# Optimization experiments

Hardware: AMD Instinct MI355X
Metric: run time of the kernel (lower is better)

Reference implementation:

```python
import jax, jax.numpy as jnp
import numpy as np

SIGMA = 0.1  # init kwarg sigma
B_CONST = 1.0  # init kwarg b
EPS = 1e-5


def setup_inputs() -> dict:
    key = jax.random.key(0)
    k1, k2 = jax.random.split(key)
    shape = (4, 256, 48, 48)  # N, C, H, W
    return {
        "featureT": jax.random.normal(k1, shape, dtype=jnp.float32),
        "featureI": jax.random.normal(k2, shape, dtype=jnp.float32),
    }


def reference(featureT, featureI):
    # center both features by the target's per-channel mean (over N, H, W)
    meanT = featureT.mean(axis=(0, 2, 3), keepdims=True)
    fI = featureI - meanT
    fT = featureT - meanT
    # l2-normalize channelwise (dim=1)
    fI = fI / jnp.linalg.norm(fI, axis=1, keepdims=True)
    fT = fT / jnp.linalg.norm(fT, axis=1, keepdims=True)
    N, C, H, W = fT.shape
    P = H * W
    # per-sample all-pairs patch cosine similarity: dist[n,p,h,w] = sum_c fT[n,c,p] * fI[n,c,h,w]
    # (equivalent to the per-sample F.conv2d with 1x1 filters from patch_decomposition)
    dist = jnp.einsum('ncp,nchw->nphw', fT.reshape(N, C, P), fI)  # [N, P, H, W]
    raw_dist = (1.0 - dist) / 2.0
    # relative distances along the patch axis (axis=1)
    div = jnp.min(raw_dist, axis=1, keepdims=True)
    relative_dist = raw_dist / (div + EPS)
    # contextual similarity: exp-weighted normalization along axis=1
    Wmat = jnp.exp((B_CONST - relative_dist) / SIGMA)
    CX = Wmat / jnp.sum(Wmat, axis=1, keepdims=True)
    # max over spatial dims (3 then 2), mean over patches
    CX = CX.max(axis=(2, 3))  # [N, P]
    CX = CX.mean(axis=1)      # [N]
    CX_B = -jnp.log(CX)       # [N]
    loss = jnp.mean(CX_B)
    return (loss, CX_B)
```

## Files before the change

### kernel.cpp

```cpp
#include <hip/hip_runtime.h>
#include <hip/hip_fp16.h>

#define NN 4
#define CC 256
#define PP 2304
#define EPSV 1e-5f

typedef __attribute__((ext_vector_type(8))) short bf16x8;
typedef __attribute__((ext_vector_type(4))) float f32x4;

struct alignas(8) h4 { __half2 a, b; };

__device__ inline unsigned fenc(float f) {
  unsigned b = __float_as_uint(f);
  return (b & 0x80000000u) ? ~b : (b | 0x80000000u);
}
__device__ inline float fdec(unsigned e) {
  unsigned b = (e & 0x80000000u) ? (e ^ 0x80000000u) : ~e;
  return __uint_as_float(b);
}

__device__ inline unsigned short f2bf(float x) {
  unsigned u = __float_as_uint(x);
  unsigned r = (u + 0x7FFFu + ((u >> 16) & 1u)) >> 16;
  return (unsigned short)r;
}

__device__ inline void gload_lds16(const unsigned short* g, unsigned short* l) {
  __builtin_amdgcn_global_load_lds(
      (const __attribute__((address_space(1))) void*)g,
      (__attribute__((address_space(3))) void*)l, 16, 0, 0);
}

__global__ __launch_bounds__(256) void k_mean(const float* __restrict__ fT,
                                              float* __restrict__ meanT,
                                              unsigned* __restrict__ divu,
                                              unsigned* __restrict__ M,
                                              float* __restrict__ cxsum) {
  int c = blockIdx.x, t = threadIdx.x;
  float s = 0.f;
  for (int n = 0; n < NN; n++) {
    const float* base = fT + (size_t)n * CC * PP + (size_t)c * PP;
    for (int p = t; p < PP; p += 256) s += base[p];
  }
  for (int o = 32; o > 0; o >>= 1) s += __shfl_down(s, o);
  __shared__ float red[4];
  if ((t & 63) == 0) red[t >> 6] = s;
  __syncthreads();
  if (t == 0) meanT[c] = (red[0] + red[1] + red[2] + red[3]) / (float)(NN * PP);
  if (t < 36) {
    int idx = c * 36 + t;
    divu[idx] = 0xFFFFFFFFu;
    M[idx] = 0u;
  }
  if (blockIdx.x == 0 && t < 4) cxsum[t] = 0.f;
}

__global__ __launch_bounds__(256) void k_norm(const float* __restrict__ fT,
                                              const float* __restrict__ fI,
                                              const float* __restrict__ meanT,
                                              unsigned short* __restrict__ A,
                                              unsigned short* __restrict__ B) {
  int n = blockIdx.y;
  int p0 = blockIdx.x * 16;
  int t = threadIdx.x;
  int tc = t >> 4, tp = t & 15;
  __shared__ float cT[16][257];
  __shared__ float cI[16][257];
  __shared__ float redT[16][17], redI[16][17];
  __shared__ float inv[2][16];
  float aT = 0.f, aI = 0.f;
  int p = p0 + tp;
  for (int c0 = 0; c0 < CC; c0 += 16) {
    int c = c0 + tc;
    float m = meanT[c];
    size_t g = (size_t)n * CC * PP + (size_t)c * PP + p;
    float vT = fT[g] - m;
    float vI = fI[g] - m;
    cT[tp][c] = vT; cI[tp][c] = vI;
    aT += vT * vT; aI += vI * vI;
  }
  redT[tp][tc] = aT; redI[tp][tc] = aI;
  __syncthreads();
  if (t < 16) {
    float sT = 0.f, sI = 0.f;
    for (int k = 0; k < 16; k++) { sT += redT[t][k]; sI += redI[t][k]; }
    inv[0][t] = 1.0f / sqrtf(sT);
    inv[1][t] = 1.0f / sqrtf(sI);
  }
  __syncthreads();
#pragma unroll
  for (int it = 0; it < 2; it++) {
    int task = it * 256 + t;
    int ps = task >> 5;
    int ch = task & 31;
    float iA = inv[0][ps], iB = inv[1][ps];
    unsigned short va[8], vb[8];
#pragma unroll
    for (int e = 0; e < 8; e++) {
      va[e] = f2bf(cT[ps][ch * 8 + e] * iA);
      vb[e] = f2bf(cI[ps][ch * 8 + e] * iB);
    }
    size_t o = ((size_t)(n * PP + p0 + ps)) * CC + ch * 8;
    *(int4*)(A + o) = *(const int4*)va;
    *(int4*)(B + o) = *(const int4*)vb;
  }
}

__global__ __launch_bounds__(256) void k_gemm(const unsigned short* __restrict__ A,
                                              const unsigned short* __restrict__ B,
                                              __half* __restrict__ rawt,
                                              unsigned* __restrict__ divu) {
  int n  = blockIdx.z;
  int i0 = blockIdx.y * 128;
  int j0 = blockIdx.x * 128;
  int t  = threadIdx.x;
  int lane = t & 63;
  int w = t >> 6;
  int wi = w >> 1, wj = w & 1;
  int lr = lane & 15, lq = lane >> 4;

  __shared__ __align__(16) char smem[33792];
  unsigned short* As = (unsigned short*)smem;
  unsigned short* Bs = (unsigned short*)(smem + 16384);
  __half* r16t = (__half*)smem;
  __shared__ unsigned cmin[128];
  if (t < 128) cmin[t] = 0xFFFFFFFFu;

  f32x4 acc[4][4];
#pragma unroll
  for (int a = 0; a < 4; a++)
#pragma unroll
    for (int b = 0; b < 4; b++) acc[a][b] = (f32x4){0.f, 0.f, 0.f, 0.f};

  const size_t baseA = ((size_t)(n * PP + i0)) * CC;
  const size_t baseB = ((size_t)(n * PP + j0)) * CC;
  int lrow8 = lane >> 3;
  int lseg  = (lane & 7) ^ (lrow8 & 7);

  for (int k0 = 0; k0 < CC; k0 += 64) {
    if (k0) __syncthreads();
#pragma unroll
    for (int it = 0; it < 4; it++) {
      int sb = (w * 4 + it) * 64;
      int row = (w * 4 + it) * 8 + lrow8;
      gload_lds16(A + baseA + (size_t)row * CC + k0 + lseg * 8, As + sb * 8);
      gload_lds16(B + baseB + (size_t)row * CC + k0 + lseg * 8, Bs + sb * 8);
    }
    __syncthreads();
#pragma unroll
    for (int ks = 0; ks < 2; ks++) {
      bf16x8 af[4], bf[4];
#pragma unroll
      for (int ti = 0; ti < 4; ti++) {
        int row = wi * 64 + ti * 16 + lr;
        int slot = row * 8 + ((ks * 4 + lq) ^ (lr & 7));
        af[ti] = *(const bf16x8*)&As[slot * 8];
      }
#pragma unroll
      for (int tj = 0; tj < 4; tj++) {
        int row = wj * 64 + tj * 16 + lr;
        int slot = row * 8 + ((ks * 4 + lq) ^ (lr & 7));
        bf[tj] = *(const bf16x8*)&Bs[slot * 8];
      }
#pragma unroll
      for (int ti = 0; ti < 4; ti++)
#pragma unroll
        for (int tj = 0; tj < 4; tj++)
          acc[ti][tj] = __builtin_amdgcn_mfma_f32_16x16x32_bf16(af[ti], bf[tj], acc[ti][tj], 0, 0, 0);
    }
  }

  __syncthreads();
#pragma unroll
  for (int tj = 0; tj < 4; tj++) {
    float mx = -1e30f;
    int cj = wj * 64 + tj * 16 + lr;
#pragma unroll
    for (int ti = 0; ti < 4; ti++) {
      alignas(8) unsigned short pk[4];
#pragma unroll
      for (int r = 0; r < 4; r++) {
        float g = acc[ti][tj][r];
        mx = fmaxf(mx, g);
        pk[r] = __half_as_ushort(__float2half((1.0f - g) * 0.5f));
      }
      int ci = wi * 64 + ti * 16 + lq * 4;
      *(short4*)&r16t[cj * 132 + ci] = *(const short4*)pk;
    }
    atomicMin(&cmin[cj], fenc((1.0f - mx) * 0.5f));
  }
  __syncthreads();
#pragma unroll
  for (int m = 0; m < 8; m++) {
    int chunk = m * 256 + t;
    int row = chunk >> 4, cs = chunk & 15;
    int2 lo = *(const int2*)&r16t[row * 132 + cs * 8];
    int2 hi = *(const int2*)&r16t[row * 132 + cs * 8 + 4];
    int4 v = {lo.x, lo.y, hi.x, hi.y};
    *(int4*)(rawt + ((size_t)(n * PP + j0 + row)) * PP + i0 + cs * 8) = v;
  }
  if (t < 128) atomicMin(&divu[n * PP + j0 + t], cmin[t]);
}

__global__ __launch_bounds__(256) void k_colsum(const __half* __restrict__ rawt,
                                                const unsigned* __restrict__ divu,
                                                float* __restrict__ S) {
  int t = threadIdx.x, lane = t & 63, w = t >> 6;
  int r = blockIdx.x * 4 + w;
  float d = fdec(divu[r]);
  float sc = -10.0f / (d + EPSV);
  const __half* rp = rawt + (size_t)r * PP;
  float s = 0.f;
#pragma unroll
  for (int c = 0; c < 9; c++) {
    h4 hv = *(const h4*)(rp + c * 256 + lane * 4);
    float2 f01 = __half22float2(hv.a);
    float2 f23 = __half22float2(hv.b);
    s += __expf(f01.x * sc) + __expf(f01.y * sc) + __expf(f23.x * sc) + __expf(f23.y * sc);
  }
  for (int o = 32; o > 0; o >>= 1) s += __shfl_down(s, o);
  if (lane == 0) S[r] = s;
}

__global__ __launch_bounds__(256) void k_logscale(const unsigned* __restrict__ divu,
                                                  const float* __restrict__ S,
                                                  float* __restrict__ scale,
                                                  float* __restrict__ lnS) {
  int i = blockIdx.x * 256 + threadIdx.x;
  float d = fdec(divu[i]);
  scale[i] = -10.0f / (d + EPSV);
  lnS[i] = logf(S[i]);
}

__global__ __launch_bounds__(256) void k_rowmax(const __half* __restrict__ rawt,
                                                const float* __restrict__ scale,
                                                const float* __restrict__ lnS,
                                                unsigned* __restrict__ M) {
  int n = blockIdx.y;
  int i0 = blockIdx.x * 256;
  int rz = blockIdx.z;
  int t = threadIdx.x;
  int lane = t & 63, w = t >> 6;
  int i = i0 + lane * 4;

  float4 m = {-1e30f, -1e30f, -1e30f, -1e30f};
  int j0 = rz * 96;
  for (int j = j0 + w; j < j0 + 96; j += 4) {
    float scj = scale[n * PP + j];
    float lsj = lnS[n * PP + j];
    h4 hv = *(const h4*)(rawt + ((size_t)(n * PP + j)) * PP + i);
    float2 f01 = __half22float2(hv.a);
    float2 f23 = __half22float2(hv.b);
    m.x = fmaxf(m.x, fmaf(f01.x, scj, -lsj));
    m.y = fmaxf(m.y, fmaf(f01.y, scj, -lsj));
    m.z = fmaxf(m.z, fmaf(f23.x, scj, -lsj));
    m.w = fmaxf(m.w, fmaf(f23.y, scj, -lsj));
  }
  __shared__ float4 red4[4][64];
  red4[w][lane] = m;
  __syncthreads();
  if (t < 64) {
    float4 a = red4[0][t], b = red4[1][t], c = red4[2][t], d = red4[3][t];
    int ii = i0 + t * 4;
    atomicMax(&M[n * PP + ii + 0], fenc(fmaxf(fmaxf(a.x, b.x), fmaxf(c.x, d.x))));
    atomicMax(&M[n * PP + ii + 1], fenc(fmaxf(fmaxf(a.y, b.y), fmaxf(c.y, d.y))));
    atomicMax(&M[n * PP + ii + 2], fenc(fmaxf(fmaxf(a.z, b.z), fmaxf(c.z, d.z))));
    atomicMax(&M[n * PP + ii + 3], fenc(fmaxf(fmaxf(a.w, b.w), fmaxf(c.w, d.w))));
  }
}

__global__ __launch_bounds__(256) void k_cx(const unsigned* __restrict__ M,
                                            float* __restrict__ cxsum) {
  int b = blockIdx.x, t = threadIdx.x;
  int idx = b * 256 + t;
  int n = idx / PP;
  float v = __expf(fdec(M[idx])) * (1.0f / (float)PP);
  for (int o = 32; o > 0; o >>= 1) v += __shfl_down(v, o);
  __shared__ float red[4];
  if ((t & 63) == 0) red[t >> 6] = v;
  __syncthreads();
  if (t == 0) atomicAdd(&cxsum[n], red[0] + red[1] + red[2] + red[3]);
}

__global__ void k_final(const float* __restrict__ cxsum, float* __restrict__ out) {
  int t = threadIdx.x;
  float cxb = 0.f;
  if (t < 4) {
    cxb = -logf(cxsum[t]);
    out[1 + t] = cxb;
  }
  for (int o = 2; o > 0; o >>= 1) cxb += __shfl_down(cxb, o);
  if (t == 0) out[0] = cxb * 0.25f;
}

extern "C" void kernel_launch(void* const* d_in, const int* in_sizes, int n_in,
                              void* d_out, int out_size, void* d_ws, size_t ws_size,
                              hipStream_t stream) {
  const float* fT = (const float*)d_in[0];
  const float* fI = (const float*)d_in[1];
  float* out = (float*)d_out;

  char* w = (char*)d_ws;
  float* meanT   = (float*)w;
  unsigned* divu = (unsigned*)(w + 1024);
  float* S       = (float*)(w + 1024 + 36864);
  float* scale   = (float*)(w + 1024 + 2 * 36864);
  float* lnS     = (float*)(w + 1024 + 3 * 36864);
  unsigned* M    = (unsigned*)(w + 1024 + 4 * 36864);
  float* cxsum   = (float*)(w + 1024 + 5 * 36864);
  size_t off = 1024 + 5 * 36864 + 1024;
  unsigned short* A = (unsigned short*)(w + off);
  unsigned short* B = (unsigned short*)(w + off + 4718592);
  __half* rawt = (__half*)(w + off + 2 * 4718592);

  k_mean<<<256, 256, 0, stream>>>(fT, meanT, divu, M, cxsum);
  k_norm<<<dim3(PP / 16, NN), 256, 0, stream>>>(fT, fI, meanT, A, B);
  k_gemm<<<dim3(PP / 128, PP / 128, NN), 256, 0, stream>>>(A, B, rawt, divu);
  k_colsum<<<dim3(PP * NN / 4), 256, 0, stream>>>(rawt, divu, S);
  k_logscale<<<36, 256, 0, stream>>>(divu, S, scale, lnS);
  k_rowmax<<<dim3(PP / 256, NN, 24), 256, 0, stream>>>(rawt, scale, lnS, M);
  k_cx<<<36, 256, 0, stream>>>(M, cxsum);
  k_final<<<1, 64, 0, stream>>>(cxsum, out);
}
```

Baseline: 131.0 us.

## Fuse logscale into colsum and rowmax with cx, vectorize mean/norm loads

Splits the mean reduction across N and C blocks with float4 loads, and has the normalization kernel sum the partials itself. It also vectorizes the norm kernel's loads along the patch axis. The separate logscale and cx kernels are folded into colsum and rowmax, and rowmax now covers the full j range per block, so the global atomicMax buffer is no longer needed. This removes two launches and an atomic-heavy pass, at the cost of less j-parallelism and more per-block work in rowmax.

```diff
diff --git a/kernel.cpp b/kernel.cpp
--- a/kernel.cpp
+++ b/kernel.cpp
@@ -33,60 +33,67 @@
 }
 
 __global__ __launch_bounds__(256) void k_mean(const float* __restrict__ fT,
-                                              float* __restrict__ meanT,
+                                              float* __restrict__ partial,
                                               unsigned* __restrict__ divu,
-                                              unsigned* __restrict__ M,
                                               float* __restrict__ cxsum) {
-  int c = blockIdx.x, t = threadIdx.x;
+  int c = blockIdx.x, n = blockIdx.y, t = threadIdx.x;
+  const float4* base = (const float4*)(fT + ((size_t)n * CC + c) * PP);
   float s = 0.f;
-  for (int n = 0; n < NN; n++) {
-    const float* base = fT + (size_t)n * CC * PP + (size_t)c * PP;
-    for (int p = t; p < PP; p += 256) s += base[p];
+  for (int k = t; k < 576; k += 256) {
+    float4 v = base[k];
+    s += (v.x + v.y) + (v.z + v.w);
   }
   for (int o = 32; o > 0; o >>= 1) s += __shfl_down(s, o);
   __shared__ float red[4];
   if ((t & 63) == 0) red[t >> 6] = s;
   __syncthreads();
-  if (t == 0) meanT[c] = (red[0] + red[1] + red[2] + red[3]) / (float)(NN * PP);
-  if (t < 36) {
-    int idx = c * 36 + t;
-    divu[idx] = 0xFFFFFFFFu;
-    M[idx] = 0u;
-  }
-  if (blockIdx.x == 0 && t < 4) cxsum[t] = 0.f;
+  if (t == 0) partial[c * NN + n] = red[0] + red[1] + red[2] + red[3];
+  if (n == 0 && t < 36) divu[c * 36 + t] = 0xFFFFFFFFu;
+  if (n == 0 && c == 0 && t < 4) cxsum[t] = 0.f;
 }
 
 __global__ __launch_bounds__(256) void k_norm(const float* __restrict__ fT,
                                               const float* __restrict__ fI,
-                                              const float* __restrict__ meanT,
+                                              const float* __restrict__ partial,
                                               unsigned short* __restrict__ A,
                                               unsigned short* __restrict__ B) {
   int n = blockIdx.y;
   int p0 = blockIdx.x * 16;
   int t = threadIdx.x;
-  int tc = t >> 4, tp = t & 15;
+  int pq = (t & 3) * 4;
+  int cg = t >> 2;
   __shared__ float cT[16][257];
   __shared__ float cI[16][257];
-  __shared__ float redT[16][17], redI[16][17];
+  __shared__ float redf[2][16][65];
   __shared__ float inv[2][16];
-  float aT = 0.f, aI = 0.f;
-  int p = p0 + tp;
-  for (int c0 = 0; c0 < CC; c0 += 16) {
-    int c = c0 + tc;
-    float m = meanT[c];
-    size_t g = (size_t)n * CC * PP + (size_t)c * PP + p;
-    float vT = fT[g] - m;
-    float vI = fI[g] - m;
-    cT[tp][c] = vT; cI[tp][c] = vI;
-    aT += vT * vT; aI += vI * vI;
-  }
-  redT[tp][tc] = aT; redI[tp][tc] = aI;
-  __syncthreads();
-  if (t < 16) {
-    float sT = 0.f, sI = 0.f;
-    for (int k = 0; k < 16; k++) { sT += redT[t][k]; sI += redI[t][k]; }
-    inv[0][t] = 1.0f / sqrtf(sT);
-    inv[1][t] = 1.0f / sqrtf(sI);
+  float aT[4] = {0.f, 0.f, 0.f, 0.f}, aI[4] = {0.f, 0.f, 0.f, 0.f};
+#pragma unroll
+  for (int ph = 0; ph < 4; ph++) {
+    int c = ph * 64 + cg;
+    float m = (partial[c * NN + 0] + partial[c * NN + 1] +
+               partial[c * NN + 2] + partial[c * NN + 3]) * (1.0f / (float)(NN * PP));
+    size_t g = ((size_t)n * CC + c) * PP + p0 + pq;
+    float4 vT = *(const float4*)(fT + g);
+    float4 vI = *(const float4*)(fI + g);
+    float xT[4] = {vT.x - m, vT.y - m, vT.z - m, vT.w - m};
+    float xI[4] = {vI.x - m, vI.y - m, vI.z - m, vI.w - m};
+#pragma unroll
+    for (int k = 0; k < 4; k++) {
+      cT[pq + k][c] = xT[k]; cI[pq + k][c] = xI[k];
+      aT[k] += xT[k] * xT[k]; aI[k] += xI[k] * xI[k];
+    }
+  }
+#pragma unroll
+  for (int k = 0; k < 4; k++) {
+    redf[0][pq + k][cg] = aT[k];
+    redf[1][pq + k][cg] = aI[k];
+  }
+  __syncthreads();
+  if (t < 32) {
+    int which = t >> 4, p = t & 15;
+    float s = 0.f;
+    for (int g = 0; g < 64; g++) s += redf[which][p][g];
+    inv[which][p] = 1.0f / sqrtf(s);
   }
   __syncthreads();
 #pragma unroll
@@ -205,7 +212,8 @@
 
 __global__ __launch_bounds__(256) void k_colsum(const __half* __restrict__ rawt,
                                                 const unsigned* __restrict__ divu,
-                                                float* __restrict__ S) {
+                                                float* __restrict__ scale,
+                                                float* __restrict__ lnS) {
   int t = threadIdx.x, lane = t & 63, w = t >> 6;
   int r = blockIdx.x * 4 + w;
   float d = fdec(divu[r]);
@@ -220,67 +228,60 @@
     s += __expf(f01.x * sc) + __expf(f01.y * sc) + __expf(f23.x * sc) + __expf(f23.y * sc);
   }
   for (int o = 32; o > 0; o >>= 1) s += __shfl_down(s, o);
-  if (lane == 0) S[r] = s;
-}
-
-__global__ __launch_bounds__(256) void k_logscale(const unsigned* __restrict__ divu,
-                                                  const float* __restrict__ S,
-                                                  float* __restrict__ scale,
-                                                  float* __restrict__ lnS) {
-  int i = blockIdx.x * 256 + threadIdx.x;
-  float d = fdec(divu[i]);
-  scale[i] = -10.0f / (d + EPSV);
-  lnS[i] = logf(S[i]);
-}
-
-__global__ __launch_bounds__(256) void k_rowmax(const __half* __restrict__ rawt,
+  if (lane == 0) {
+    scale[r] = sc;
+    lnS[r] = logf(s);
+  }
+}
+
+__global__ __launch_bounds__(512) void k_rowmax(const __half* __restrict__ rawt,
                                                 const float* __restrict__ scale,
                                                 const float* __restrict__ lnS,
-                                                unsigned* __restrict__ M) {
+                                                float* __restrict__ cxsum) {
   int n = blockIdx.y;
-  int i0 = blockIdx.x * 256;
-  int rz = blockIdx.z;
-  int t = threadIdx.x;
-  int lane = t & 63, w = t >> 6;
-  int i = i0 + lane * 4;
-
-  float4 m = {-1e30f, -1e30f, -1e30f, -1e30f};
-  int j0 = rz * 96;
-  for (int j = j0 + w; j < j0 + 96; j += 4) {
-    float scj = scale[n * PP + j];
-    float lsj = lnS[n * PP + j];
+  int i0 = blockIdx.x * 32;
+  int t = threadIdx.x, lane = t & 63, w = t >> 6;
+  int q = t & 7, g = t >> 3;
+  int i = i0 + q * 4;
+  const float* scp = scale + n * PP;
+  const float* lnp = lnS + n * PP;
+  float m0 = -1e30f, m1 = -1e30f, m2 = -1e30f, m3 = -1e30f;
+#pragma unroll 4
+  for (int it = 0; it < 36; it++) {
+    int j = it * 64 + g;
+    float scj = scp[j], lsj = lnp[j];
     h4 hv = *(const h4*)(rawt + ((size_t)(n * PP + j)) * PP + i);
     float2 f01 = __half22float2(hv.a);
     float2 f23 = __half22float2(hv.b);
-    m.x = fmaxf(m.x, fmaf(f01.x, scj, -lsj));
-    m.y = fmaxf(m.y, fmaf(f01.y, scj, -lsj));
-    m.z = fmaxf(m.z, fmaf(f23.x, scj, -lsj));
-    m.w = fmaxf(m.w, fmaf(f23.y, scj, -lsj));
-  }
-  __shared__ float4 red4[4][64];
-  red4[w][lane] = m;
-  __syncthreads();
-  if (t < 64) {
-    float4 a = red4[0][t], b = red4[1][t], c = red4[2][t], d = red4[3][t];
-    int ii = i0 + t * 4;
-    atomicMax(&M[n * PP + ii + 0], fenc(fmaxf(fmaxf(a.x, b.x), fmaxf(c.x, d.x))));
-    atomicMax(&M[n * PP + ii + 1], fenc(fmaxf(fmaxf(a.y, b.y), fmaxf(c.y, d.y))));
-    atomicMax(&M[n * PP + ii + 2], fenc(fmaxf(fmaxf(a.z, b.z), fmaxf(c.z, d.z))));
-    atomicMax(&M[n * PP + ii + 3], fenc(fmaxf(fmaxf(a.w, b.w), fmaxf(c.w, d.w))));
-  }
-}
-
-__global__ __launch_bounds__(256) void k_cx(const unsigned* __restrict__ M,
-                                            float* __restrict__ cxsum) {
-  int b = blockIdx.x, t = threadIdx.x;
-  int idx = b * 256 + t;
-  int n = idx / PP;
-  float v = __expf(fdec(M[idx])) * (1.0f / (float)PP);
-  for (int o = 32; o > 0; o >>= 1) v += __shfl_down(v, o);
-  __shared__ float red[4];
-  if ((t & 63) == 0) red[t >> 6] = v;
-  __syncthreads();
-  if (t == 0) atomicAdd(&cxsum[n], red[0] + red[1] + red[2] + red[3]);
+    m0 = fmaxf(m0, fmaf(f01.x, scj, -lsj));
+    m1 = fmaxf(m1, fmaf(f01.y, scj, -lsj));
+    m2 = fmaxf(m2, fmaf(f23.x, scj, -lsj));
+    m3 = fmaxf(m3, fmaf(f23.y, scj, -lsj));
+  }
+#pragma unroll
+  for (int o = 8; o <= 32; o <<= 1) {
+    m0 = fmaxf(m0, __shfl_xor(m0, o));
+    m1 = fmaxf(m1, __shfl_xor(m1, o));
+    m2 = fmaxf(m2, __shfl_xor(m2, o));
+    m3 = fmaxf(m3, __shfl_xor(m3, o));
+  }
+  __shared__ float4 red[8][8];
+  if (lane < 8) red[w][lane] = (float4){m0, m1, m2, m3};
+  __syncthreads();
+  if (t < 8) {
+    float4 a = red[0][t];
+#pragma unroll
+    for (int ww = 1; ww < 8; ww++) {
+      float4 b = red[ww][t];
+      a.x = fmaxf(a.x, b.x); a.y = fmaxf(a.y, b.y);
+      a.z = fmaxf(a.z, b.z); a.w = fmaxf(a.w, b.w);
+    }
+    float v = (__expf(a.x) + __expf(a.y) + __expf(a.z) + __expf(a.w)) * (1.0f / (float)PP);
+    v += __shfl_down(v, 4);
+    v += __shfl_down(v, 2);
+    v += __shfl_down(v, 1);
+    if (t == 0) atomicAdd(&cxsum[n], v);
+  }
 }
 
 __global__ void k_final(const float* __restrict__ cxsum, float* __restrict__ out) {
@@ -302,24 +303,20 @@
   float* out = (float*)d_out;
 
   char* w = (char*)d_ws;
-  float* meanT   = (float*)w;
-  unsigned* divu = (unsigned*)(w + 1024);
-  float* S       = (float*)(w + 1024 + 36864);
-  float* scale   = (float*)(w + 1024 + 2 * 36864);
-  float* lnS     = (float*)(w + 1024 + 3 * 36864);
-  unsigned* M    = (unsigned*)(w + 1024 + 4 * 36864);
-  float* cxsum   = (float*)(w + 1024 + 5 * 36864);
-  size_t off = 1024 + 5 * 36864 + 1024;
+  float* partial = (float*)w;
+  unsigned* divu = (unsigned*)(w + 4096);
+  float* scale   = (float*)(w + 4096 + 36864);
+  float* lnS     = (float*)(w + 4096 + 2 * 36864);
+  float* cxsum   = (float*)(w + 4096 + 3 * 36864);
+  size_t off = 4096 + 3 * 36864 + 1024;
   unsigned short* A = (unsigned short*)(w + off);
   unsigned short* B = (unsigned short*)(w + off + 4718592);
   __half* rawt = (__half*)(w + off + 2 * 4718592);
 
-  k_mean<<<256, 256, 0, stream>>>(fT, meanT, divu, M, cxsum);
-  k_norm<<<dim3(PP / 16, NN), 256, 0, stream>>>(fT, fI, meanT, A, B);
+  k_mean<<<dim3(CC, NN), 256, 0, stream>>>(fT, partial, divu, cxsum);
+  k_norm<<<dim3(PP / 16, NN), 256, 0, stream>>>(fT, fI, partial, A, B);
   k_gemm<<<dim3(PP / 128, PP / 128, NN), 256, 0, stream>>>(A, B, rawt, divu);
-  k_colsum<<<dim3(PP * NN / 4), 256, 0, stream>>>(rawt, divu, S);
-  k_logscale<<<36, 256, 0, stream>>>(divu, S, scale, lnS);
-  k_rowmax<<<dim3(PP / 256, NN, 24), 256, 0, stream>>>(rawt, scale, lnS, M);
-  k_cx<<<36, 256, 0, stream>>>(M, cxsum);
+  k_colsum<<<dim3(PP * NN / 4), 256, 0, stream>>>(rawt, divu, scale, lnS);
+  k_rowmax<<<dim3(PP / 32, NN), 512, 0, stream>>>(rawt, scale, lnS, cxsum);
   k_final<<<1, 64, 0, stream>>>(cxsum, out);
 }
```

Result: faster. 126.6 us (-3.4%).
